# Performance work log

Hardware: AMD Instinct MI355X
Metric: run time of the kernel (lower is better)

Reference implementation:

```python
import jax, jax.numpy as jnp
import numpy as np

N = 2048      # nodes
E = 65536     # edges (avg degree 32)
NV = 6        # n_views (edge_attr dim)
C1, C2, C3 = 32, 32, 32


def _nnconv(x, edge_index, edge_attr, W, b, root, bias, in_c, out_c):
    # Edge MLP: Linear(n_views, in*out) + ReLU -> per-edge weight matrix [E, in, out]
    w = jax.nn.relu(edge_attr @ W + b).reshape(-1, in_c, out_c)
    src, dst = edge_index[0], edge_index[1]  # source_to_target flow
    msg = jnp.einsum('ei,eio->eo', x[src], w)          # gather + edge-specific matmul
    summed = jax.ops.segment_sum(msg, dst, num_segments=N)
    cnt = jax.ops.segment_sum(jnp.ones((msg.shape[0],), x.dtype), dst, num_segments=N)
    agg = summed / jnp.maximum(cnt, 1.0)[:, None]       # scatter-mean (0 for isolated nodes)
    return agg + x @ root + bias                        # root weight + bias (PyG NNConv defaults)


def setup_inputs() -> dict:
    key = jax.random.key(0)
    ks = jax.random.split(key, 12)
    s = 0.1
    return {
        'x': jax.random.normal(ks[0], (N, 1), jnp.float32),
        'edge_attr': jax.random.uniform(ks[1], (E, NV), jnp.float32),
        'edge_index': jax.random.randint(ks[2], (2, E), 0, N, jnp.int64),
        'W1': jax.random.normal(ks[3], (NV, 1 * C1), jnp.float32) * s,
        'b1': jnp.zeros((1 * C1,), jnp.float32),
        'root1': jax.random.normal(ks[4], (1, C1), jnp.float32) * s,
        'bias1': jnp.zeros((C1,), jnp.float32),
        'W2': jax.random.normal(ks[5], (NV, C1 * C2), jnp.float32) * s,
        'b2': jnp.zeros((C1 * C2,), jnp.float32),
        'root2': jax.random.normal(ks[6], (C1, C2), jnp.float32) * s,
        'bias2': jnp.zeros((C2,), jnp.float32),
        'W3': jax.random.normal(ks[7], (NV, C2 * C3), jnp.float32) * s,
        'b3': jnp.zeros((C2 * C3,), jnp.float32),
        'root3': jax.random.normal(ks[8], (C2, C3), jnp.float32) * s,
        'bias3': jnp.zeros((C3,), jnp.float32),
    }


def reference(x, edge_attr, edge_index, W1, b1, root1, bias1, W2, b2, root2, bias2, W3, b3, root3, bias3):
    h = jax.nn.relu(_nnconv(x, edge_index, edge_attr, W1, b1, root1, bias1, 1, C1))
    h = jax.nn.relu(_nnconv(h, edge_index, edge_attr, W2, b2, root2, bias2, C1, C2))
    h = jax.nn.relu(_nnconv(h, edge_index, edge_attr, W3, b3, root3, bias3, C2, C3))
    # CBT: cbt[i, j] = sum_k |h[j, k] - h[i, k]|  (all-pairs L1 distance, [N, N])
    cbt = jnp.sum(jnp.abs(h[None, :, :] - h[:, None, :]), axis=2)
    return cbt
```

## Files before the change

kernel.cpp:

```cpp
#include <hip/hip_runtime.h>

#define N_NODES 2048
#define N_EDGES 65536
#define NV 6
#define C 32


__global__ void edge1_kernel(const float* __restrict__ x,
                             const float* __restrict__ ea,
                             const int* __restrict__ src,
                             const int* __restrict__ dst,
                             const float* __restrict__ W1,
                             const float* __restrict__ b1,
                             float* __restrict__ sum1,
                             float* __restrict__ cnt) {
    int t = blockIdx.x * blockDim.x + threadIdx.x;
    int e = t >> 5, o = t & 31;
    if (e >= N_EDGES) return;
    const float* eap = ea + e * NV;
    float w = b1[o];
#pragma unroll
    for (int v = 0; v < NV; v++) w = fmaf(eap[v], W1[v * C + o], w);
    w = fmaxf(w, 0.0f);
    int d = dst[e];
    atomicAdd(&sum1[d * C + o], x[src[e]] * w);
    if (o == 0) atomicAdd(&cnt[d], 1.0f);
}

template <int IN_C>
__global__ void node_kernel(const float* __restrict__ sum,
                            const float* __restrict__ cnt,
                            const float* __restrict__ hprev,
                            const float* __restrict__ root,
                            const float* __restrict__ bias,
                            float* __restrict__ hout) {
    int t = blockIdx.x * blockDim.x + threadIdx.x;
    int n = t >> 5, o = t & 31;
    float inv = 1.0f / fmaxf(cnt[n], 1.0f);
    float acc = sum[t] * inv + bias[o];
#pragma unroll
    for (int i = 0; i < IN_C; i++) acc = fmaf(hprev[n * IN_C + i], root[i * C + o], acc);
    hout[t] = fmaxf(acc, 0.0f);
}

__global__ __launch_bounds__(256) void edge23_kernel(
    const float* __restrict__ hprev,
    const float* __restrict__ ea,
    const int* __restrict__ src,
    const int* __restrict__ dst,
    const float* __restrict__ W,
    const float* __restrict__ b,
    float* __restrict__ sumout)
{
    __shared__ float hb[4][256];
    const int lane = threadIdx.x & 63;
    const int o = lane & 31;
    const int half = lane >> 5;
    const int i0 = half * 16;
    const int w = threadIdx.x >> 6;
    float* hbw = &hb[w][0];

    float wreg[16][6], breg[16];
#pragma unroll
    for (int j = 0; j < 16; j++) {
#pragma unroll
        for (int v = 0; v < 6; v++) wreg[j][v] = W[v * 1024 + (i0 + j) * C + o];
        breg[j] = b[(i0 + j) * C + o];
    }

    const int wid = (blockIdx.x * 256 + threadIdx.x) >> 6;
    for (int g = wid; g < N_EDGES / 8; g += 2048) {
        const int e0 = g * 8;
        const int4 sq = *(const int4*)&src[e0 + half * 4];
        float4 hq;
        hq.x = hprev[sq.x * C + o];
        hq.y = hprev[sq.y * C + o];
        hq.z = hprev[sq.z * C + o];
        hq.w = hprev[sq.w * C + o];
        *(float4*)&hbw[half * 128 + o * 4] = hq;

        float accs[8];
        const float4* eap4 = (const float4*)(ea + (size_t)e0 * NV);
#pragma unroll
        for (int sub = 0; sub < 2; sub++) {
            float eaf[24];
#pragma unroll
            for (int t = 0; t < 6; t++) *(float4*)&eaf[t * 4] = eap4[sub * 6 + t];
            float a0 = 0.0f, a1 = 0.0f, a2 = 0.0f, a3 = 0.0f;
#pragma unroll
            for (int j = 0; j < 16; j++) {
                const float4 hA = *(const float4*)&hbw[sub * 128 + (i0 + j) * 4];
                const float bb = breg[j];
                const float w0 = wreg[j][0], w1 = wreg[j][1], w2 = wreg[j][2];
                const float w3 = wreg[j][3], w4 = wreg[j][4], w5 = wreg[j][5];
                float t0 = bb, t1 = bb, t2 = bb, t3 = bb;
                t0 = fmaf(eaf[0],  w0, t0); t1 = fmaf(eaf[6],  w0, t1);
                t2 = fmaf(eaf[12], w0, t2); t3 = fmaf(eaf[18], w0, t3);
                t0 = fmaf(eaf[1],  w1, t0); t1 = fmaf(eaf[7],  w1, t1);
                t2 = fmaf(eaf[13], w1, t2); t3 = fmaf(eaf[19], w1, t3);
                t0 = fmaf(eaf[2],  w2, t0); t1 = fmaf(eaf[8],  w2, t1);
                t2 = fmaf(eaf[14], w2, t2); t3 = fmaf(eaf[20], w2, t3);
                t0 = fmaf(eaf[3],  w3, t0); t1 = fmaf(eaf[9],  w3, t1);
                t2 = fmaf(eaf[15], w3, t2); t3 = fmaf(eaf[21], w3, t3);
                t0 = fmaf(eaf[4],  w4, t0); t1 = fmaf(eaf[10], w4, t1);
                t2 = fmaf(eaf[16], w4, t2); t3 = fmaf(eaf[22], w4, t3);
                t0 = fmaf(eaf[5],  w5, t0); t1 = fmaf(eaf[11], w5, t1);
                t2 = fmaf(eaf[17], w5, t2); t3 = fmaf(eaf[23], w5, t3);
                a0 = fmaf(hA.x, fmaxf(t0, 0.0f), a0);
                a1 = fmaf(hA.y, fmaxf(t1, 0.0f), a1);
                a2 = fmaf(hA.z, fmaxf(t2, 0.0f), a2);
                a3 = fmaf(hA.w, fmaxf(t3, 0.0f), a3);
            }
            accs[sub * 4 + 0] = a0; accs[sub * 4 + 1] = a1;
            accs[sub * 4 + 2] = a2; accs[sub * 4 + 3] = a3;
        }
#pragma unroll
        for (int k = 0; k < 8; k++) accs[k] += __shfl_down(accs[k], 32);

        const int4 dA = *(const int4*)&dst[e0];
        const int4 dB = *(const int4*)&dst[e0 + 4];
        if (lane < 32) {
            atomicAdd(&sumout[dA.x * C + o], accs[0]);
            atomicAdd(&sumout[dA.y * C + o], accs[1]);
            atomicAdd(&sumout[dA.z * C + o], accs[2]);
            atomicAdd(&sumout[dA.w * C + o], accs[3]);
            atomicAdd(&sumout[dB.x * C + o], accs[4]);
            atomicAdd(&sumout[dB.y * C + o], accs[5]);
            atomicAdd(&sumout[dB.z * C + o], accs[6]);
            atomicAdd(&sumout[dB.w * C + o], accs[7]);
        }
    }
}

__global__ __launch_bounds__(256) void cbt_kernel(const float* __restrict__ h,
                                                  float* __restrict__ out) {
    __shared__ float hj_s[64][33];
    __shared__ float hi_s[64 * 32];
    const int lane = threadIdx.x & 63;
    const int w = threadIdx.x >> 6;
    const int j0 = blockIdx.x * 64;
    const int i0 = blockIdx.y * 64;
    for (int t = threadIdx.x; t < 64 * 32; t += 256) {
        hj_s[t >> 5][t & 31] = h[j0 * 32 + t];
        hi_s[t] = h[i0 * 32 + t];
    }
    __syncthreads();
    float hj[32];
#pragma unroll
    for (int k = 0; k < 32; k++) hj[k] = hj_s[lane][k];
    const int j = j0 + lane;
#pragma unroll 4
    for (int ii = w * 16; ii < w * 16 + 16; ii++) {
        float acc = 0.0f;
#pragma unroll
        for (int k = 0; k < 32; k++) {
            acc += fabsf(hi_s[ii * 32 + k] - hj[k]);
        }
        out[(size_t)(i0 + ii) * N_NODES + j] = acc;
    }
}

extern "C" void kernel_launch(void* const* d_in, const int* in_sizes, int n_in,
                              void* d_out, int out_size, void* d_ws, size_t ws_size,
                              hipStream_t stream) {
    const float* x         = (const float*)d_in[0];
    const float* edge_attr = (const float*)d_in[1];
    const int*   edge_idx  = (const int*)d_in[2];
    const float* W1 = (const float*)d_in[3];
    const float* b1 = (const float*)d_in[4];
    const float* root1 = (const float*)d_in[5];
    const float* bias1 = (const float*)d_in[6];
    const float* W2 = (const float*)d_in[7];
    const float* b2 = (const float*)d_in[8];
    const float* root2 = (const float*)d_in[9];
    const float* bias2 = (const float*)d_in[10];
    const float* W3 = (const float*)d_in[11];
    const float* b3 = (const float*)d_in[12];
    const float* root3 = (const float*)d_in[13];
    const float* bias3 = (const float*)d_in[14];

    const int* src = edge_idx;
    const int* dst = edge_idx + N_EDGES;

    float* ws   = (float*)d_ws;
    float* cnt  = ws;
    float* sum1 = ws + N_NODES;
    float* sum2 = sum1 + N_NODES * C;
    float* sum3 = sum2 + N_NODES * C;
    float* h1   = sum3 + N_NODES * C;
    float* h2   = h1 + N_NODES * C;
    float* h3   = h2 + N_NODES * C;

    hipMemsetAsync(d_ws, 0, (size_t)(N_NODES + 3 * N_NODES * C) * sizeof(float), stream);

    edge1_kernel<<<(N_EDGES * C) / 256, 256, 0, stream>>>(x, edge_attr, src, dst, W1, b1, sum1, cnt);
    node_kernel<1><<<(N_NODES * C) / 256, 256, 0, stream>>>(sum1, cnt, x, root1, bias1, h1);

    edge23_kernel<<<512, 256, 0, stream>>>(h1, edge_attr, src, dst, W2, b2, sum2);
    node_kernel<C><<<(N_NODES * C) / 256, 256, 0, stream>>>(sum2, cnt, h1, root2, bias2, h2);

    edge23_kernel<<<512, 256, 0, stream>>>(h2, edge_attr, src, dst, W3, b3, sum3);
    node_kernel<C><<<(N_NODES * C) / 256, 256, 0, stream>>>(sum3, cnt, h2, root3, bias3, h3);

    cbt_kernel<<<dim3(N_NODES / 64, N_NODES / 64), 256, 0, stream>>>(h3, (float*)d_out);
}
```

Before: 168.5 us.

## Replace atomic scatter-add with CSR build and per-node gather aggregation

Builds a CSR index by destination (histogram, scan, scatter), then computes layer 1 per node and writes layer 2/3 edge messages to a buffer that a per-node gather kernel sums, fused with the root matmul, bias and ReLU. This removes float atomics and the separate node kernels. In exchange it adds three setup kernels, an 8 MB message buffer round-trip through memory per layer, and random gathers. Edge order within each node is set by atomics, so summation order is nondeterministic.

```diff
diff --git a/kernel.cpp b/kernel.cpp
--- a/kernel.cpp
+++ b/kernel.cpp
@@ -4,53 +4,88 @@
 #define N_EDGES 65536
 #define NV 6
 #define C 32
-
-
-__global__ void edge1_kernel(const float* __restrict__ x,
-                             const float* __restrict__ ea,
-                             const int* __restrict__ src,
-                             const int* __restrict__ dst,
-                             const float* __restrict__ W1,
-                             const float* __restrict__ b1,
-                             float* __restrict__ sum1,
-                             float* __restrict__ cnt) {
-    int t = blockIdx.x * blockDim.x + threadIdx.x;
-    int e = t >> 5, o = t & 31;
-    if (e >= N_EDGES) return;
-    const float* eap = ea + e * NV;
-    float w = b1[o];
-#pragma unroll
-    for (int v = 0; v < NV; v++) w = fmaf(eap[v], W1[v * C + o], w);
-    w = fmaxf(w, 0.0f);
-    int d = dst[e];
-    atomicAdd(&sum1[d * C + o], x[src[e]] * w);
-    if (o == 0) atomicAdd(&cnt[d], 1.0f);
-}
-
-template <int IN_C>
-__global__ void node_kernel(const float* __restrict__ sum,
-                            const float* __restrict__ cnt,
-                            const float* __restrict__ hprev,
-                            const float* __restrict__ root,
-                            const float* __restrict__ bias,
-                            float* __restrict__ hout) {
-    int t = blockIdx.x * blockDim.x + threadIdx.x;
-    int n = t >> 5, o = t & 31;
-    float inv = 1.0f / fmaxf(cnt[n], 1.0f);
-    float acc = sum[t] * inv + bias[o];
-#pragma unroll
-    for (int i = 0; i < IN_C; i++) acc = fmaf(hprev[n * IN_C + i], root[i * C + o], acc);
-    hout[t] = fmaxf(acc, 0.0f);
-}
-
-__global__ __launch_bounds__(256) void edge23_kernel(
+#define BLK 256
+
+
+__global__ void hist_kernel(const int* __restrict__ dst, int* __restrict__ cnt) {
+    int e = blockIdx.x * blockDim.x + threadIdx.x;
+    if (e < N_EDGES) atomicAdd(&cnt[dst[e]], 1);
+}
+
+__global__ __launch_bounds__(256) void scan_kernel(const int* __restrict__ cnt,
+                                                   int* __restrict__ rowptr) {
+    __shared__ int part[256];
+    const int tid = threadIdx.x;
+    int local[8];
+    int s = 0;
+#pragma unroll
+    for (int k = 0; k < 8; k++) { local[k] = cnt[tid * 8 + k]; s += local[k]; }
+    part[tid] = s;
+    __syncthreads();
+    for (int off = 1; off < 256; off <<= 1) {
+        int v = (tid >= off) ? part[tid - off] : 0;
+        __syncthreads();
+        part[tid] += v;
+        __syncthreads();
+    }
+    int run = part[tid] - s;
+#pragma unroll
+    for (int k = 0; k < 8; k++) { rowptr[tid * 8 + k] = run; run += local[k]; }
+    if (tid == 255) rowptr[2048] = run;
+}
+
+__global__ void scatter_kernel(const int* __restrict__ dst, const int* __restrict__ rowptr,
+                               int* __restrict__ cursor, int* __restrict__ eid) {
+    int e = blockIdx.x * blockDim.x + threadIdx.x;
+    if (e < N_EDGES) {
+        int d = dst[e];
+        int pos = atomicAdd(&cursor[d], 1);
+        eid[rowptr[d] + pos] = e;
+    }
+}
+
+__global__ __launch_bounds__(BLK) void layer1_kernel(
+    const float* __restrict__ x, const float* __restrict__ ea,
+    const int* __restrict__ src, const int* __restrict__ rowptr,
+    const int* __restrict__ eid,
+    const float* __restrict__ W1, const float* __restrict__ b1,
+    const float* __restrict__ root1, const float* __restrict__ bias1,
+    float* __restrict__ h1) {
+    const int lane = threadIdx.x & 63;
+    const int o = lane & 31;
+    const int p = lane >> 5;
+    const int n = blockIdx.x * 4 + (threadIdx.x >> 6);
+    float w1r[NV];
+#pragma unroll
+    for (int v = 0; v < NV; v++) w1r[v] = W1[v * C + o];
+    const float b1o = b1[o];
+    const int beg = rowptr[n], end = rowptr[n + 1];
+    float acc = 0.0f;
+    for (int k = beg + p; k < end; k += 2) {
+        const int e = eid[k];
+        const float xs = x[src[e]];
+        const float* eap = ea + e * NV;
+        float t = b1o;
+#pragma unroll
+        for (int v = 0; v < NV; v++) t = fmaf(eap[v], w1r[v], t);
+        acc = fmaf(xs, fmaxf(t, 0.0f), acc);
+    }
+    acc += __shfl_down(acc, 32);
+    if (lane < 32) {
+        const float inv = 1.0f / fmaxf((float)(end - beg), 1.0f);
+        float r = fmaf(acc, inv, bias1[o]);
+        r = fmaf(x[n], root1[o], r);
+        h1[n * C + o] = fmaxf(r, 0.0f);
+    }
+}
+
+__global__ __launch_bounds__(BLK) void edge23_kernel(
     const float* __restrict__ hprev,
     const float* __restrict__ ea,
     const int* __restrict__ src,
-    const int* __restrict__ dst,
     const float* __restrict__ W,
     const float* __restrict__ b,
-    float* __restrict__ sumout)
+    float* __restrict__ msg)
 {
     __shared__ float hb[4][256];
     const int lane = threadIdx.x & 63;
@@ -68,7 +103,7 @@
         breg[j] = b[(i0 + j) * C + o];
     }
 
-    const int wid = (blockIdx.x * 256 + threadIdx.x) >> 6;
+    const int wid = (blockIdx.x * BLK + threadIdx.x) >> 6;
     for (int g = wid; g < N_EDGES / 8; g += 2048) {
         const int e0 = g * 8;
         const int4 sq = *(const int4*)&src[e0 + half * 4];
@@ -116,23 +151,47 @@
         }
 #pragma unroll
         for (int k = 0; k < 8; k++) accs[k] += __shfl_down(accs[k], 32);
-
-        const int4 dA = *(const int4*)&dst[e0];
-        const int4 dB = *(const int4*)&dst[e0 + 4];
         if (lane < 32) {
-            atomicAdd(&sumout[dA.x * C + o], accs[0]);
-            atomicAdd(&sumout[dA.y * C + o], accs[1]);
-            atomicAdd(&sumout[dA.z * C + o], accs[2]);
-            atomicAdd(&sumout[dA.w * C + o], accs[3]);
-            atomicAdd(&sumout[dB.x * C + o], accs[4]);
-            atomicAdd(&sumout[dB.y * C + o], accs[5]);
-            atomicAdd(&sumout[dB.z * C + o], accs[6]);
-            atomicAdd(&sumout[dB.w * C + o], accs[7]);
+            float* mp = msg + (size_t)e0 * C + o;
+#pragma unroll
+            for (int k = 0; k < 8; k++) mp[k * C] = accs[k];
         }
     }
 }
 
-__global__ __launch_bounds__(256) void cbt_kernel(const float* __restrict__ h,
+__global__ __launch_bounds__(BLK) void gather_kernel(
+    const float* __restrict__ msg, const int* __restrict__ rowptr,
+    const int* __restrict__ eid, const float* __restrict__ hprev,
+    const float* __restrict__ root,
+    const float* __restrict__ bias,
+    float* __restrict__ hout) {
+    const int lane = threadIdx.x & 63;
+    const int o = lane & 31;
+    const int p = lane >> 5;
+    const int n = blockIdx.x * 4 + (threadIdx.x >> 6);
+    const int beg = rowptr[n], end = rowptr[n + 1];
+    float acc = 0.0f;
+    int k = beg + p;
+    for (; k + 7 <= end; k += 8) {
+        int ka = eid[k], kb = eid[k + 2], kc = eid[k + 4], kd = eid[k + 6];
+        float m0 = msg[ka * C + o];
+        float m1 = msg[kb * C + o];
+        float m2 = msg[kc * C + o];
+        float m3 = msg[kd * C + o];
+        acc += (m0 + m1) + (m2 + m3);
+    }
+    for (; k < end; k += 2) acc += msg[eid[k] * C + o];
+    acc += __shfl_down(acc, 32);
+    if (lane < 32) {
+        const float inv = 1.0f / fmaxf((float)(end - beg), 1.0f);
+        float r = fmaf(acc, inv, bias[o]);
+#pragma unroll
+        for (int i = 0; i < C; i++) r = fmaf(hprev[n * C + i], root[i * C + o], r);
+        hout[n * C + o] = fmaxf(r, 0.0f);
+    }
+}
+
+__global__ __launch_bounds__(BLK) void cbt_kernel(const float* __restrict__ h,
                                                   float* __restrict__ out) {
     __shared__ float hj_s[64][33];
     __shared__ float hi_s[64 * 32];
@@ -140,7 +199,7 @@
     const int w = threadIdx.x >> 6;
     const int j0 = blockIdx.x * 64;
     const int i0 = blockIdx.y * 64;
-    for (int t = threadIdx.x; t < 64 * 32; t += 256) {
+    for (int t = threadIdx.x; t < 64 * 32; t += BLK) {
         hj_s[t >> 5][t & 31] = h[j0 * 32 + t];
         hi_s[t] = h[i0 * 32 + t];
     }
@@ -153,9 +212,7 @@
     for (int ii = w * 16; ii < w * 16 + 16; ii++) {
         float acc = 0.0f;
 #pragma unroll
-        for (int k = 0; k < 32; k++) {
-            acc += fabsf(hi_s[ii * 32 + k] - hj[k]);
-        }
+        for (int k = 0; k < 32; k++) acc += fabsf(hi_s[ii * 32 + k] - hj[k]);
         out[(size_t)(i0 + ii) * N_NODES + j] = acc;
     }
 }
@@ -182,25 +239,28 @@
     const int* src = edge_idx;
     const int* dst = edge_idx + N_EDGES;
 
-    float* ws   = (float*)d_ws;
-    float* cnt  = ws;
-    float* sum1 = ws + N_NODES;
-    float* sum2 = sum1 + N_NODES * C;
-    float* sum3 = sum2 + N_NODES * C;
-    float* h1   = sum3 + N_NODES * C;
+    int* wsi    = (int*)d_ws;
+    int* cnt_i  = wsi;
+    int* cursor = wsi + 2048;
+    int* rowptr = wsi + 4096;
+    int* eid    = wsi + 6160;
+    float* msg  = (float*)(wsi + 6160 + 65536);
+    float* h1   = msg + (size_t)N_EDGES * C;
     float* h2   = h1 + N_NODES * C;
     float* h3   = h2 + N_NODES * C;
 
-    hipMemsetAsync(d_ws, 0, (size_t)(N_NODES + 3 * N_NODES * C) * sizeof(float), stream);
-
-    edge1_kernel<<<(N_EDGES * C) / 256, 256, 0, stream>>>(x, edge_attr, src, dst, W1, b1, sum1, cnt);
-    node_kernel<1><<<(N_NODES * C) / 256, 256, 0, stream>>>(sum1, cnt, x, root1, bias1, h1);
-
-    edge23_kernel<<<512, 256, 0, stream>>>(h1, edge_attr, src, dst, W2, b2, sum2);
-    node_kernel<C><<<(N_NODES * C) / 256, 256, 0, stream>>>(sum2, cnt, h1, root2, bias2, h2);
-
-    edge23_kernel<<<512, 256, 0, stream>>>(h2, edge_attr, src, dst, W3, b3, sum3);
-    node_kernel<C><<<(N_NODES * C) / 256, 256, 0, stream>>>(sum3, cnt, h2, root3, bias3, h3);
-
-    cbt_kernel<<<dim3(N_NODES / 64, N_NODES / 64), 256, 0, stream>>>(h3, (float*)d_out);
-}
+    hipMemsetAsync(d_ws, 0, 4096 * sizeof(int), stream);
+
+    hist_kernel<<<N_EDGES / BLK, BLK, 0, stream>>>(dst, cnt_i);
+    scan_kernel<<<1, 256, 0, stream>>>(cnt_i, rowptr);
+    scatter_kernel<<<N_EDGES / BLK, BLK, 0, stream>>>(dst, rowptr, cursor, eid);
+
+    layer1_kernel<<<N_NODES / 4, BLK, 0, stream>>>(x, edge_attr, src, rowptr, eid,
+                                                   W1, b1, root1, bias1, h1);
+    edge23_kernel<<<512, BLK, 0, stream>>>(h1, edge_attr, src, W2, b2, msg);
+    gather_kernel<<<N_NODES / 4, BLK, 0, stream>>>(msg, rowptr, eid, h1, root2, bias2, h2);
+    edge23_kernel<<<512, BLK, 0, stream>>>(h2, edge_attr, src, W3, b3, msg);
+    gather_kernel<<<N_NODES / 4, BLK, 0, stream>>>(msg, rowptr, eid, h2, root3, bias3, h3);
+
+    cbt_kernel<<<dim3(N_NODES / 64, N_NODES / 64), BLK, 0, stream>>>(h3, (float*)d_out);
+}
```

After: 194.3 us. 15.3% more time.

## Prefetch all edge-group gathers up front and fold sum2/sum3 zeroing into edge1

Applied to the files above, without the earlier changes.

The edge23 kernel now replaces its strided loop with a fixed set of four edge groups per wave. It loads all src indices and gathers all hprev rows into a larger shared buffer before any compute, so the gather latency overlaps instead of stalling each iteration. The memset is shrunk to cover only cnt and sum1, and edge1 zeroes sum2/sum3 itself, removing part of a memset pass. The change hard-codes four iterations per wave, which matches the grid size exactly, and adds launch_bounds occupancy hints plus more shared memory per block.

```diff
diff --git a/kernel.cpp b/kernel.cpp
--- a/kernel.cpp
+++ b/kernel.cpp
@@ -4,6 +4,7 @@
 #define N_EDGES 65536
 #define NV 6
 #define C 32
+#define BLK 256
 
 
 __global__ void edge1_kernel(const float* __restrict__ x,
@@ -13,8 +14,10 @@
                              const float* __restrict__ W1,
                              const float* __restrict__ b1,
                              float* __restrict__ sum1,
+                             float* __restrict__ sum23,
                              float* __restrict__ cnt) {
     int t = blockIdx.x * blockDim.x + threadIdx.x;
+    if (t < 2 * N_NODES * C) sum23[t] = 0.0f;
     int e = t >> 5, o = t & 31;
     if (e >= N_EDGES) return;
     const float* eap = ea + e * NV;
@@ -43,7 +46,7 @@
     hout[t] = fmaxf(acc, 0.0f);
 }
 
-__global__ __launch_bounds__(256) void edge23_kernel(
+__global__ __launch_bounds__(BLK, 2) void edge23_kernel(
     const float* __restrict__ hprev,
     const float* __restrict__ ea,
     const int* __restrict__ src,
@@ -52,13 +55,12 @@
     const float* __restrict__ b,
     float* __restrict__ sumout)
 {
-    __shared__ float hb[4][256];
+    __shared__ float hb[4][4][256];
     const int lane = threadIdx.x & 63;
     const int o = lane & 31;
     const int half = lane >> 5;
     const int i0 = half * 16;
     const int w = threadIdx.x >> 6;
-    float* hbw = &hb[w][0];
 
     float wreg[16][6], breg[16];
 #pragma unroll
@@ -68,19 +70,28 @@
         breg[j] = b[(i0 + j) * C + o];
     }
 
-    const int wid = (blockIdx.x * 256 + threadIdx.x) >> 6;
-    for (int g = wid; g < N_EDGES / 8; g += 2048) {
-        const int e0 = g * 8;
-        const int4 sq = *(const int4*)&src[e0 + half * 4];
+    const int wid = (blockIdx.x * BLK + threadIdx.x) >> 6;
+
+    int4 sqs[4];
+#pragma unroll
+    for (int i = 0; i < 4; i++)
+        sqs[i] = *(const int4*)&src[(wid + i * 2048) * 8 + half * 4];
+#pragma unroll
+    for (int i = 0; i < 4; i++) {
         float4 hq;
-        hq.x = hprev[sq.x * C + o];
-        hq.y = hprev[sq.y * C + o];
-        hq.z = hprev[sq.z * C + o];
-        hq.w = hprev[sq.w * C + o];
-        *(float4*)&hbw[half * 128 + o * 4] = hq;
-
+        hq.x = hprev[sqs[i].x * C + o];
+        hq.y = hprev[sqs[i].y * C + o];
+        hq.z = hprev[sqs[i].z * C + o];
+        hq.w = hprev[sqs[i].w * C + o];
+        *(float4*)&hb[w][i][half * 128 + o * 4] = hq;
+    }
+
+#pragma unroll 2
+    for (int i = 0; i < 4; i++) {
+        const int e0 = (wid + i * 2048) * 8;
+        const float* hbw = &hb[w][i][0];
+        const float4* eap4 = (const float4*)(ea + (size_t)e0 * NV);
         float accs[8];
-        const float4* eap4 = (const float4*)(ea + (size_t)e0 * NV);
 #pragma unroll
         for (int sub = 0; sub < 2; sub++) {
             float eaf[24];
@@ -132,7 +143,7 @@
     }
 }
 
-__global__ __launch_bounds__(256) void cbt_kernel(const float* __restrict__ h,
+__global__ __launch_bounds__(BLK) void cbt_kernel(const float* __restrict__ h,
                                                   float* __restrict__ out) {
     __shared__ float hj_s[64][33];
     __shared__ float hi_s[64 * 32];
@@ -140,7 +151,7 @@
     const int w = threadIdx.x >> 6;
     const int j0 = blockIdx.x * 64;
     const int i0 = blockIdx.y * 64;
-    for (int t = threadIdx.x; t < 64 * 32; t += 256) {
+    for (int t = threadIdx.x; t < 64 * 32; t += BLK) {
         hj_s[t >> 5][t & 31] = h[j0 * 32 + t];
         hi_s[t] = h[i0 * 32 + t];
     }
@@ -153,9 +164,7 @@
     for (int ii = w * 16; ii < w * 16 + 16; ii++) {
         float acc = 0.0f;
 #pragma unroll
-        for (int k = 0; k < 32; k++) {
-            acc += fabsf(hi_s[ii * 32 + k] - hj[k]);
-        }
+        for (int k = 0; k < 32; k++) acc += fabsf(hi_s[ii * 32 + k] - hj[k]);
         out[(size_t)(i0 + ii) * N_NODES + j] = acc;
     }
 }
@@ -191,16 +200,17 @@
     float* h2   = h1 + N_NODES * C;
     float* h3   = h2 + N_NODES * C;
 
-    hipMemsetAsync(d_ws, 0, (size_t)(N_NODES + 3 * N_NODES * C) * sizeof(float), stream);
-
-    edge1_kernel<<<(N_EDGES * C) / 256, 256, 0, stream>>>(x, edge_attr, src, dst, W1, b1, sum1, cnt);
-    node_kernel<1><<<(N_NODES * C) / 256, 256, 0, stream>>>(sum1, cnt, x, root1, bias1, h1);
-
-    edge23_kernel<<<512, 256, 0, stream>>>(h1, edge_attr, src, dst, W2, b2, sum2);
-    node_kernel<C><<<(N_NODES * C) / 256, 256, 0, stream>>>(sum2, cnt, h1, root2, bias2, h2);
-
-    edge23_kernel<<<512, 256, 0, stream>>>(h2, edge_attr, src, dst, W3, b3, sum3);
-    node_kernel<C><<<(N_NODES * C) / 256, 256, 0, stream>>>(sum3, cnt, h2, root3, bias3, h3);
-
-    cbt_kernel<<<dim3(N_NODES / 64, N_NODES / 64), 256, 0, stream>>>(h3, (float*)d_out);
-}
+    hipMemsetAsync(d_ws, 0, (size_t)(N_NODES + N_NODES * C) * sizeof(float), stream);
+
+    edge1_kernel<<<(N_EDGES * C) / BLK, BLK, 0, stream>>>(x, edge_attr, src, dst,
+                                                          W1, b1, sum1, sum2, cnt);
+    node_kernel<1><<<(N_NODES * C) / BLK, BLK, 0, stream>>>(sum1, cnt, x, root1, bias1, h1);
+
+    edge23_kernel<<<512, BLK, 0, stream>>>(h1, edge_attr, src, dst, W2, b2, sum2);
+    node_kernel<C><<<(N_NODES * C) / BLK, BLK, 0, stream>>>(sum2, cnt, h1, root2, bias2, h2);
+
+    edge23_kernel<<<512, BLK, 0, stream>>>(h2, edge_attr, src, dst, W3, b3, sum3);
+    node_kernel<C><<<(N_NODES * C) / BLK, BLK, 0, stream>>>(sum3, cnt, h2, root3, bias3, h3);
+
+    cbt_kernel<<<dim3(N_NODES / 64, N_NODES / 64), BLK, 0, stream>>>(h3, (float*)d_out);
+}
```

New measurement: 166.6 us (median of 3 runs). About the same (-1.1%).
